# Performance work log

Hardware: AMD Instinct MI355X
Metric: run time of the kernel (lower is better)

## Reference

```python
import jax, jax.numpy as jnp
import numpy as np

DEGREE = 3
N_BASIS = 16


def _clamped_knots(n_basis, degree):
    # Clamped uniform knot vector on [0, 1]: degree+1 repeated knots at each end.
    n_interior = n_basis - degree - 1
    interior = np.linspace(0.0, 1.0, n_interior + 2)[1:-1]
    knots = np.concatenate([np.zeros(degree + 1), interior, np.ones(degree + 1)])
    return jnp.asarray(knots, dtype=jnp.float32)


def bspline_basis(x, degree=DEGREE, n_basis=N_BASIS):
    # Cox-de Boor recursion, vectorized over all leading dims of x.
    # x: (...,) in [0,1] -> (..., n_basis)
    t = _clamped_knots(n_basis, degree)
    n_knots = n_basis + degree + 1
    xe = jnp.clip(x, 0.0, 1.0 - 1e-6)[..., None]
    B = ((xe >= t[:-1]) & (xe < t[1:])).astype(x.dtype)  # (..., n_knots-1)
    for p in range(1, degree + 1):
        dl = t[p:n_knots - 1] - t[:n_knots - 1 - p]
        dr = t[p + 1:n_knots] - t[1:n_knots - p]
        left = jnp.where(dl > 0, (xe - t[:n_knots - 1 - p]) / jnp.where(dl > 0, dl, 1.0), 0.0)
        right = jnp.where(dr > 0, (t[p + 1:n_knots] - xe) / jnp.where(dr > 0, dr, 1.0), 0.0)
        B = left * B[..., :-1] + right * B[..., 1:]
    return B  # (..., n_basis)


def _kl(cm, lv):
    # KL(N(cm, exp(lv)) || N(0, 1)) summed over all edges/coeffs (prior_scale = 1).
    var = jnp.exp(lv)
    return 0.5 * jnp.sum(var + cm * cm - 1.0 - lv)


def _layer(x, cm, lv):
    # x: (B, in); cm, lv: (out, in, n_basis)
    basis = bspline_basis(x)  # (B, in, n_basis)
    out = jnp.einsum('bik,oik->bo', basis, cm)  # fused per-edge weighted sum
    return out, _kl(cm, lv)


def setup_inputs() -> dict:
    key = jax.random.key(0)
    ks = jax.random.split(key, 4)
    B = 8192
    sizes = [256, 512, 512, 256]
    nb = N_BASIS
    inp = {"x": jax.random.uniform(ks[0], (B, sizes[0]), dtype=jnp.float32)}
    for i in range(3):
        inp[f"cm{i}"] = 0.1 * jax.random.normal(ks[1 + i], (sizes[i + 1], sizes[i], nb), dtype=jnp.float32)
        inp[f"lv{i}"] = -2.0 * jnp.ones((sizes[i + 1], sizes[i], nb), dtype=jnp.float32)
    return inp


def reference(x, cm0, lv0, cm1, lv1, cm2, lv2):
    out = x
    kl = jnp.zeros((), x.dtype)
    for cm, lv in ((cm0, lv0), (cm1, lv1), (cm2, lv2)):
        out, k = _layer(out, cm, lv)
        kl = kl + k
    return out, kl
```

## Files before the change

kernel.cpp:

```cpp
#include <hip/hip_runtime.h>
#include <hip/hip_bf16.h>


typedef __attribute__((ext_vector_type(8))) _Float16 f16x8;
typedef __attribute__((ext_vector_type(4))) float float4v;
typedef unsigned short ushort_t;

__device__ __forceinline__ ushort_t f2h(float f) {
  _Float16 h = (_Float16)f;
  return *(ushort_t*)&h;
}
__device__ __forceinline__ float h2f(ushort_t u) {
  return (float)*(_Float16*)&u;
}

__device__ __forceinline__ void bspline_w4(float x, int& k0, float w[4]) {
  const float XMAX = 1.0f - 1e-6f;
  float xe = fminf(fmaxf(x, 0.0f), XMAX);
  int cell = (int)(xe * 13.0f);
  cell = cell > 12 ? 12 : cell;
  k0 = cell;
  int j = cell + 3;
  const float s = 1.0f / 13.0f;
  int cjm2 = max(j - 5, 0);
  int cjm1 = max(j - 4, 0);
  int cj   = j - 3;
  int cj1  = j - 2;
  int cj2  = min(j - 1, 13);
  int cj3  = min(j, 13);
  float tjm1 = cjm1 * s, tj = cj * s;
  float tjm2 = cjm2 * s;
  float tj1 = cj1 * s, tj2 = cj2 * s, tj3 = cj3 * s;
  float left1 = xe - tj, left2 = xe - tjm1, left3 = xe - tjm2;
  float right1 = tj1 - xe, right2 = tj2 - xe, right3 = tj3 - xe;
#define INV3(d) ((d) == 1 ? 13.0f : ((d) == 2 ? 6.5f : (13.0f / 3.0f)))
  float i10 = INV3(cj1 - cj);
  float i20 = INV3(cj1 - cjm1), i21 = INV3(cj2 - cj);
  float i30 = INV3(cj1 - cjm2), i31 = INV3(cj2 - cjm1), i32 = INV3(cj3 - cj);
#undef INV3
  float temp = i10;
  float N0 = right1 * temp;
  float N1 = left1 * temp;
  temp = N0 * i20;
  N0 = right1 * temp;
  float saved = left2 * temp;
  temp = N1 * i21;
  N1 = saved + right2 * temp;
  float N2 = left1 * temp;
  temp = N0 * i30;
  N0 = right1 * temp;
  saved = left3 * temp;
  temp = N1 * i31;
  N1 = saved + right2 * temp;
  saved = left2 * temp;
  temp = N2 * i32;
  N2 = saved + right3 * temp;
  float N3 = left1 * temp;
  w[0] = N0; w[1] = N1; w[2] = N2; w[3] = N3;
}

template <bool SPLIT_A>
__global__ __launch_bounds__(256, 4) void kan_layer(
    const float* __restrict__ act, const ushort_t* __restrict__ Bsw,
    float* __restrict__ outp, int IN, int OUT) {
  const int K = IN * 16;
  const int KC = K >> 3;
  __shared__ ushort_t Ah[2][64 * 72];
  __shared__ ushort_t Al[SPLIT_A ? 2 : 1][SPLIT_A ? 64 * 72 : 1];

  const int tid = threadIdx.x;
  const int lane = tid & 63;
  const int wn = tid >> 6;
  const int quad = lane >> 4, l15 = lane & 15;
  const int b0 = blockIdx.x * 64;
  const int n0 = blockIdx.y * 128;
  const int tbase = (n0 >> 4) + wn * 2;

  float4v acc[4][2];
#pragma unroll
  for (int a = 0; a < 4; a++)
#pragma unroll
    for (int b = 0; b < 2; b++) acc[a][b] = (float4v)0.0f;

  const int gm = tid >> 2;
  const int gf = tid & 3;
  const float* xrow = &act[(size_t)(b0 + gm) * IN + gf];

  const ushort_t* bbase[2];
#pragma unroll
  for (int nt = 0; nt < 2; ++nt)
    bbase[nt] = Bsw + (size_t)(tbase + nt) * KC * 128 + lane * 8;

  const int nsteps = K / 64;
  const int chunk = nsteps / gridDim.z;
  const int kbeg = blockIdx.z * chunk;
  const int kend = kbeg + chunk;
  const int klast = kend - 1;

#define EVAL_WRITE(BUF, XS)                                                   \
  {                                                                           \
    int k0a; float wa[4];                                                     \
    bspline_w4(XS, k0a, wa);                                                  \
    uint4 z4; z4.x = z4.y = z4.z = z4.w = 0u;                                 \
    ushort_t* arow_h = &Ah[BUF][gm * 72 + gf * 16];                           \
    ((uint4*)arow_h)[0] = z4; ((uint4*)arow_h)[1] = z4;                       \
    _Pragma("unroll")                                                         \
    for (int t = 0; t < 4; ++t) arow_h[k0a + t] = f2h(wa[t]);                 \
    if (SPLIT_A) {                                                            \
      ushort_t* arow_l = &Al[BUF][gm * 72 + gf * 16];                         \
      ((uint4*)arow_l)[0] = z4; ((uint4*)arow_l)[1] = z4;                     \
      _Pragma("unroll")                                                       \
      for (int t = 0; t < 4; ++t)                                             \
        arow_l[k0a + t] = f2h(wa[t] - h2f(f2h(wa[t])));                       \
    }                                                                         \
  }

#define MFMA_STEP(BUF, BF)                                                    \
  _Pragma("unroll")                                                           \
  for (int ks = 0; ks < 2; ++ks) {                                            \
    f16x8 ahf[4], alf[4];                                                     \
    _Pragma("unroll")                                                         \
    for (int mt = 0; mt < 4; ++mt) {                                          \
      int off = (mt * 16 + l15) * 72 + ks * 32 + quad * 8;                    \
      ahf[mt] = *(const f16x8*)&Ah[BUF][off];                                 \
      if (SPLIT_A) alf[mt] = *(const f16x8*)&Al[BUF][off];                    \
    }                                                                         \
    _Pragma("unroll")                                                         \
    for (int mt = 0; mt < 4; ++mt)                                            \
      _Pragma("unroll")                                                       \
      for (int nt = 0; nt < 2; ++nt) {                                        \
        if (SPLIT_A)                                                          \
          acc[mt][nt] = __builtin_amdgcn_mfma_f32_16x16x32_f16(               \
              alf[mt], (BF)[ks][nt], acc[mt][nt], 0, 0, 0);                   \
        acc[mt][nt] = __builtin_amdgcn_mfma_f32_16x16x32_f16(                 \
            ahf[mt], (BF)[ks][nt], acc[mt][nt], 0, 0, 0);                     \
      }                                                                       \
  }

#define KSTEP_BODY(KS, CUR, BFC, BFN, XVC, XVN)                               \
  {                                                                           \
    const int kp1 = ((KS) + 1 <= klast) ? (KS) + 1 : klast;                   \
    const int kp2 = ((KS) + 2 <= klast) ? (KS) + 2 : klast;                   \
    _Pragma("unroll")                                                         \
    for (int ks = 0; ks < 2; ++ks)                                            \
      _Pragma("unroll")                                                       \
      for (int nt = 0; nt < 2; ++nt)                                          \
        BFN[ks][nt] =                                                         \
            *(const f16x8*)&bbase[nt][(size_t)kp1 * 1024 + ks * 512];         \
    XVN = xrow[kp2 * 4];                                                      \
    MFMA_STEP(CUR, BFC);                                                      \
    EVAL_WRITE((CUR) ^ 1, XVC);                                               \
    __syncthreads();                                                          \
  }

  f16x8 bf0[2][2], bf1[2][2];
#pragma unroll
  for (int ks = 0; ks < 2; ++ks)
#pragma unroll
    for (int nt = 0; nt < 2; ++nt)
      bf0[ks][nt] = *(const f16x8*)&bbase[nt][(size_t)kbeg * 1024 + ks * 512];
  float xvP = xrow[kbeg * 4];
  float xv0 = xrow[((kbeg + 1 <= klast) ? kbeg + 1 : klast) * 4];
  float xv1;
  EVAL_WRITE(0, xvP);
  __syncthreads();

  for (int k = kbeg; k < kend; k += 2) {
    KSTEP_BODY(k,     0, bf0, bf1, xv0, xv1);
    KSTEP_BODY(k + 1, 1, bf1, bf0, xv1, xv0);
  }

#undef KSTEP_BODY
#undef MFMA_STEP
#undef EVAL_WRITE

#pragma unroll
  for (int mt = 0; mt < 4; ++mt)
#pragma unroll
    for (int nt = 0; nt < 2; ++nt) {
      int col = n0 + wn * 32 + nt * 16 + l15;
#pragma unroll
      for (int r = 0; r < 4; ++r) {
        int row = b0 + mt * 16 + quad * 4 + r;
        atomicAdd(&outp[(size_t)row * OUT + col], acc[mt][nt][r]);
      }
    }
}

__global__ __launch_bounds__(256) void kl_convert(
    const float* __restrict__ cm, const float* __restrict__ lv,
    ushort_t* __restrict__ bsw, int G ,
    long long ngroups, float* __restrict__ klout) {
  long long i = (long long)blockIdx.x * blockDim.x + threadIdx.x;
  const long long stride = (long long)gridDim.x * blockDim.x;
  float s = 0.0f;
  for (; i < ngroups; i += stride) {
    int o = (int)(i / G);
    int kc = (int)(i - (long long)o * G);
    const float* cp = &cm[i * 8];
    const float* lp = &lv[i * 8];
    unsigned pk[4];
#pragma unroll
    for (int t = 0; t < 4; ++t) {
      float c0 = cp[2 * t], c1 = cp[2 * t + 1];
      float l0 = lp[2 * t], l1 = lp[2 * t + 1];
      pk[t] = (unsigned)f2h(c0) | ((unsigned)f2h(c1) << 16);
      s += 0.5f * (__expf(l0) + c0 * c0 - 1.0f - l0);
      s += 0.5f * (__expf(l1) + c1 * c1 - 1.0f - l1);
    }
    uint4 v; v.x = pk[0]; v.y = pk[1]; v.z = pk[2]; v.w = pk[3];
    size_t doff = (((size_t)(o >> 4) * G + kc) * 16 + (o & 15)) * 8;
    *(uint4*)&bsw[doff] = v;
  }
#pragma unroll
  for (int off = 32; off > 0; off >>= 1) s += __shfl_down(s, off, 64);
  __shared__ float red[4];
  int wv = threadIdx.x >> 6;
  if ((threadIdx.x & 63) == 0) red[wv] = s;
  __syncthreads();
  if (threadIdx.x == 0)
    atomicAdd(klout, red[0] + red[1] + red[2] + red[3]);
}

extern "C" void kernel_launch(void* const* d_in, const int* in_sizes, int n_in,
                              void* d_out, int out_size, void* d_ws, size_t ws_size,
                              hipStream_t stream) {
  const float* x   = (const float*)d_in[0];
  const float* cm0 = (const float*)d_in[1];
  const float* lv0 = (const float*)d_in[2];
  const float* cm1 = (const float*)d_in[3];
  const float* lv1 = (const float*)d_in[4];
  const float* cm2 = (const float*)d_in[5];
  const float* lv2 = (const float*)d_in[6];

  float* out = (float*)d_out;
  float* klp = out + (size_t)8192 * 256;

  char* ws = (char*)d_ws;
  float*    act1 = (float*)(ws);
  float*    act2 = (float*)(ws + ((size_t)16 << 20));
  ushort_t* b0sw = (ushort_t*)(ws + ((size_t)32 << 20));
  ushort_t* b1sw = (ushort_t*)(ws + ((size_t)36 << 20));
  ushort_t* b2sw = (ushort_t*)(ws + ((size_t)44 << 20));

  hipMemsetAsync(ws, 0, (size_t)32 << 20, stream);
  hipMemsetAsync(d_out, 0, (size_t)out_size * sizeof(float), stream);

  kl_convert<<<2048, 256, 0, stream>>>(cm0, lv0, b0sw, 256 * 2, 512LL * 256 * 2, klp);
  kl_convert<<<2048, 256, 0, stream>>>(cm1, lv1, b1sw, 512 * 2, 512LL * 512 * 2, klp);
  kl_convert<<<2048, 256, 0, stream>>>(cm2, lv2, b2sw, 512 * 2, 256LL * 512 * 2, klp);

  kan_layer<true ><<<dim3(128, 4, 4), 256, 0, stream>>>(x,    b0sw, act1, 256, 512);
  kan_layer<false><<<dim3(128, 4, 4), 256, 0, stream>>>(act1, b1sw, act2, 512, 512);
  kan_layer<false><<<dim3(128, 2, 8), 256, 0, stream>>>(act2, b2sw, out,  512, 256);
}
```

Measured before the change: 461.5 us.

## Process two K-steps per barrier with four-buffer LDS pipeline in layers 2-3

Adds a P2 template path, used for the second and third layers, that holds four LDS A buffers and four B register fragments. Each iteration runs two K-steps of MFMA and writes basis values for the next two K-steps before one barrier, which halves the number of __syncthreads. In exchange it doubles LDS for A, adds B fragment registers, and assumes the K range per block has an even length. The extra register and LDS use could lower occupancy below the launch-bounds target.

```diff
diff --git a/kernel.cpp b/kernel.cpp
--- a/kernel.cpp
+++ b/kernel.cpp
@@ -59,13 +59,13 @@
   w[0] = N0; w[1] = N1; w[2] = N2; w[3] = N3;
 }
 
-template <bool SPLIT_A>
+template <bool SPLIT_A, bool P2>
 __global__ __launch_bounds__(256, 4) void kan_layer(
     const float* __restrict__ act, const ushort_t* __restrict__ Bsw,
     float* __restrict__ outp, int IN, int OUT) {
   const int K = IN * 16;
   const int KC = K >> 3;
-  __shared__ ushort_t Ah[2][64 * 72];
+  __shared__ ushort_t Ah[P2 ? 4 : 2][64 * 72];
   __shared__ ushort_t Al[SPLIT_A ? 2 : 1][SPLIT_A ? 64 * 72 : 1];
 
   const int tid = threadIdx.x;
@@ -137,40 +137,87 @@
       }                                                                       \
   }
 
+#define LOAD_B(BF, KP)                                                        \
+  _Pragma("unroll")                                                           \
+  for (int ks = 0; ks < 2; ++ks)                                              \
+    _Pragma("unroll")                                                         \
+    for (int nt = 0; nt < 2; ++nt)                                            \
+      BF[ks][nt] = *(const f16x8*)&bbase[nt][(size_t)(KP) * 1024 + ks * 512];
+
+  f16x8 bf0[2][2], bf1[2][2];
+
+  if constexpr (!P2) {
 #define KSTEP_BODY(KS, CUR, BFC, BFN, XVC, XVN)                               \
   {                                                                           \
     const int kp1 = ((KS) + 1 <= klast) ? (KS) + 1 : klast;                   \
     const int kp2 = ((KS) + 2 <= klast) ? (KS) + 2 : klast;                   \
-    _Pragma("unroll")                                                         \
-    for (int ks = 0; ks < 2; ++ks)                                            \
-      _Pragma("unroll")                                                       \
-      for (int nt = 0; nt < 2; ++nt)                                          \
-        BFN[ks][nt] =                                                         \
-            *(const f16x8*)&bbase[nt][(size_t)kp1 * 1024 + ks * 512];         \
+    LOAD_B(BFN, kp1);                                                         \
     XVN = xrow[kp2 * 4];                                                      \
     MFMA_STEP(CUR, BFC);                                                      \
     EVAL_WRITE((CUR) ^ 1, XVC);                                               \
     __syncthreads();                                                          \
   }
-
-  f16x8 bf0[2][2], bf1[2][2];
-#pragma unroll
-  for (int ks = 0; ks < 2; ++ks)
-#pragma unroll
-    for (int nt = 0; nt < 2; ++nt)
-      bf0[ks][nt] = *(const f16x8*)&bbase[nt][(size_t)kbeg * 1024 + ks * 512];
-  float xvP = xrow[kbeg * 4];
-  float xv0 = xrow[((kbeg + 1 <= klast) ? kbeg + 1 : klast) * 4];
-  float xv1;
-  EVAL_WRITE(0, xvP);
-  __syncthreads();
-
-  for (int k = kbeg; k < kend; k += 2) {
-    KSTEP_BODY(k,     0, bf0, bf1, xv0, xv1);
-    KSTEP_BODY(k + 1, 1, bf1, bf0, xv1, xv0);
-  }
-
+    LOAD_B(bf0, kbeg);
+    float xvP = xrow[kbeg * 4];
+    float xv0 = xrow[((kbeg + 1 <= klast) ? kbeg + 1 : klast) * 4];
+    float xv1;
+    EVAL_WRITE(0, xvP);
+    __syncthreads();
+    for (int k = kbeg; k < kend; k += 2) {
+      KSTEP_BODY(k,     0, bf0, bf1, xv0, xv1);
+      KSTEP_BODY(k + 1, 1, bf1, bf0, xv1, xv0);
+    }
 #undef KSTEP_BODY
+  } else {
+    f16x8 bf2[2][2], bf3[2][2];
+    LOAD_B(bf0, kbeg);
+    LOAD_B(bf1, kbeg + 1);
+    float xvA = xrow[kbeg * 4];
+    float xvB = xrow[(kbeg + 1) * 4];
+    EVAL_WRITE(0, xvA);
+    EVAL_WRITE(1, xvB);
+    float xvC = xrow[((kbeg + 2 <= klast) ? kbeg + 2 : klast) * 4];
+    float xvD = xrow[((kbeg + 3 <= klast) ? kbeg + 3 : klast) * 4];
+    __syncthreads();
+    for (int k = kbeg; k < kend; k += 4) {
+      {
+        const int kp2 = (k + 2 <= klast) ? k + 2 : klast;
+        const int kp3 = (k + 3 <= klast) ? k + 3 : klast;
+        const int kp4 = (k + 4 <= klast) ? k + 4 : klast;
+        const int kp5 = (k + 5 <= klast) ? k + 5 : klast;
+        LOAD_B(bf2, kp2);
+        LOAD_B(bf3, kp3);
+        const float nxA = xrow[kp4 * 4];
+        const float nxB = xrow[kp5 * 4];
+        MFMA_STEP(0, bf0);
+        MFMA_STEP(1, bf1);
+        EVAL_WRITE(2, xvC);
+        EVAL_WRITE(3, xvD);
+        __syncthreads();
+        xvA = nxA; xvB = nxB;
+      }
+      {
+        const int kp4 = (k + 4 <= klast) ? k + 4 : klast;
+        const int kp5 = (k + 5 <= klast) ? k + 5 : klast;
+        const int kp6 = (k + 6 <= klast) ? k + 6 : klast;
+        const int kp7 = (k + 7 <= klast) ? k + 7 : klast;
+        LOAD_B(bf0, kp4);
+        LOAD_B(bf1, kp5);
+        const float nxC = xrow[kp6 * 4];
+        const float nxD = xrow[kp7 * 4];
+        MFMA_STEP(2, bf2);
+        MFMA_STEP(3, bf3);
+        if (k + 4 < kend) {
+          EVAL_WRITE(0, xvA);
+          EVAL_WRITE(1, xvB);
+        }
+        __syncthreads();
+        xvC = nxC; xvD = nxD;
+      }
+    }
+  }
+
+#undef LOAD_B
 #undef MFMA_STEP
 #undef EVAL_WRITE
 
@@ -250,7 +297,7 @@
   kl_convert<<<2048, 256, 0, stream>>>(cm1, lv1, b1sw, 512 * 2, 512LL * 512 * 2, klp);
   kl_convert<<<2048, 256, 0, stream>>>(cm2, lv2, b2sw, 512 * 2, 256LL * 512 * 2, klp);
 
-  kan_layer<true ><<<dim3(128, 4, 4), 256, 0, stream>>>(x,    b0sw, act1, 256, 512);
-  kan_layer<false><<<dim3(128, 4, 4), 256, 0, stream>>>(act1, b1sw, act2, 512, 512);
-  kan_layer<false><<<dim3(128, 2, 8), 256, 0, stream>>>(act2, b2sw, out,  512, 256);
-}
+  kan_layer<true , false><<<dim3(128, 4, 4), 256, 0, stream>>>(x,    b0sw, act1, 256, 512);
+  kan_layer<false, true ><<<dim3(128, 4, 4), 256, 0, stream>>>(act1, b1sw, act2, 512, 512);
+  kan_layer<false, true ><<<dim3(128, 2, 8), 256, 0, stream>>>(act2, b2sw, out,  512, 256);
+}
```

Result: slower. 494.5 us (+7.1%).
